# Kernel tuning notes

Hardware: AMD Instinct MI355X
Metric: run time of the kernel (lower is better)

Reference implementation:

```python
import jax, jax.numpy as jnp
import numpy as np

SHRINK_THRES = 0.0025
EPS = 1e-12  # F.normalize default eps


def _l2norm(v, axis=-1):
    return v / jnp.maximum(jnp.linalg.norm(v, axis=axis, keepdims=True), EPS)


def setup_inputs() -> dict:
    key = jax.random.key(0)
    ks = jax.random.split(key, 5)
    N, C, H, W = 16, 256, 64, 64
    mem_dim = 512
    x = jax.random.normal(ks[0], (N, C, H, W), dtype=jnp.float32)
    memory = jax.random.normal(ks[1], (mem_dim, C), dtype=jnp.float32) * 0.1
    memory = _l2norm(memory, axis=1)
    w1 = jax.random.normal(ks[2], (C, C // 2), dtype=jnp.float32) * (1.0 / np.sqrt(C))
    b1 = jnp.zeros((C // 2,), dtype=jnp.float32)
    w2 = jax.random.normal(ks[3], (C // 2, C), dtype=jnp.float32) * (1.0 / np.sqrt(C // 2))
    b2 = jnp.zeros((C,), dtype=jnp.float32)
    return {"x": x, "memory": memory, "w1": w1, "b1": b1, "w2": w2, "b2": b2}


def reference(x, memory, w1, b1, w2, b2):
    N, C, H, W = x.shape
    # [N,C,H,W] -> [N*H*W, C]
    x_flat = jnp.transpose(x, (0, 2, 3, 1)).reshape(-1, C)
    x_norm = _l2norm(x_flat, axis=1)
    # shared MLP over memory slots: Linear -> ReLU -> Linear -> ReLU
    m = jax.nn.relu(memory @ w1 + b1)
    m = jax.nn.relu(m @ w2 + b2)
    mem_norm = _l2norm(m, axis=1)  # [M, C]
    # cosine similarity + softmax over memory slots
    att = jax.nn.softmax(x_norm @ mem_norm.T, axis=1)  # [N*H*W, M]
    # hard shrink + L1 renormalization
    att = jax.nn.relu(att - SHRINK_THRES)
    att = att / jnp.maximum(jnp.sum(att, axis=1, keepdims=True), EPS)
    out_flat = att @ mem_norm  # [N*H*W, C]
    output = jnp.transpose(out_flat.reshape(N, H, W, C), (0, 3, 1, 2))
    att_map = jnp.transpose(att.reshape(N, H, W, -1), (0, 3, 1, 2))
    return output, att_map
```

## Files before the change

### kernel.cpp

```cpp
#include <hip/hip_runtime.h>
#include <hip/hip_bf16.h>

typedef _Float16 half8 __attribute__((ext_vector_type(8)));
typedef _Float16 half4v __attribute__((ext_vector_type(4)));
typedef float floatx4 __attribute__((ext_vector_type(4)));

#define C_DIM 256
#define M_DIM 512
#define HW 4096
#define TAU 0.0025f

__global__ __launch_bounds__(128) void prep_kernel(
    const float* __restrict__ memory, const float* __restrict__ w1,
    const float* __restrict__ b1, const float* __restrict__ w2,
    const float* __restrict__ b2,
    _Float16* __restrict__ mN, float* __restrict__ mN32)
{
  __shared__ float sm[256];
  __shared__ float sh[128];
  __shared__ float s_part[2];
  __shared__ float s_tot;
  const int r = blockIdx.x;
  const int t = threadIdx.x;
  sm[t]       = memory[r * C_DIM + t];
  sm[t + 128] = memory[r * C_DIM + t + 128];
  __syncthreads();
  float acc = b1[t];
#pragma unroll 8
  for (int c = 0; c < 256; ++c) acc = fmaf(sm[c], w1[c * 128 + t], acc);
  sh[t] = fmaxf(acc, 0.f);
  __syncthreads();
  float o0 = b2[t], o1 = b2[t + 128];
#pragma unroll 8
  for (int k = 0; k < 128; ++k) {
    float h = sh[k];
    o0 = fmaf(h, w2[k * 256 + t], o0);
    o1 = fmaf(h, w2[k * 256 + t + 128], o1);
  }
  o0 = fmaxf(o0, 0.f);
  o1 = fmaxf(o1, 0.f);
  float ss = o0 * o0 + o1 * o1;
#pragma unroll
  for (int off = 32; off >= 1; off >>= 1) ss += __shfl_down(ss, off);
  if ((t & 63) == 0) s_part[t >> 6] = ss;
  __syncthreads();
  if (t == 0) s_tot = s_part[0] + s_part[1];
  __syncthreads();
  const float inv = 1.f / fmaxf(sqrtf(s_tot), 1e-12f);
  const float v0 = o0 * inv, v1 = o1 * inv;
  mN[r * C_DIM + t]        = (_Float16)v0;
  mN[r * C_DIM + t + 128]  = (_Float16)v1;
  mN32[r * C_DIM + t]       = v0;
  mN32[r * C_DIM + t + 128] = v1;
}

#define MFMA16(a, b, c) __builtin_amdgcn_mfma_f32_16x16x32_f16(a, b, c, 0, 0, 0)

__global__ __launch_bounds__(512, 6) void main_kernel(
    const float* __restrict__ x,
    const _Float16* __restrict__ mN,
    const float* __restrict__ mN32,
    float* __restrict__ out, float* __restrict__ attmap)
{
  __shared__ _Float16 Xh[32][264];
  __shared__ int      s_lslot[32][120];
  __shared__ float    s_lval[32][120];
  __shared__ int      s_cnt[32];
  __shared__ float    s_sumsq[32];
  __shared__ float    s_sum1[32];
  __shared__ float    s_sum2[32];

  const int tid  = threadIdx.x;
  const int wave = tid >> 6;
  const int lane = tid & 63;
  const int q    = lane >> 4;
  const int c16  = lane & 15;
  const int g    = tid >> 3;
  const int pxq  = tid & 7;

  const int blk = blockIdx.x;
  const int img = blk >> 7;
  const int hw0 = (blk & 127) * 32;
  const float* __restrict__ xb = x + (size_t)img * C_DIM * HW + hw0;

  if (tid < 32) {
    s_sumsq[tid] = 0.f; s_sum1[tid] = 0.f; s_sum2[tid] = 0.f; s_cnt[tid] = 0;
  }
  __syncthreads();

  {
    floatx4 v[4];
#pragma unroll
    for (int i = 0; i < 4; ++i)
      v[i] = *(const floatx4*)(xb + (size_t)(4 * g + i) * HW + pxq * 4);
    float ps[4];
#pragma unroll
    for (int j = 0; j < 4; ++j) {
      const int p = pxq * 4 + j;
      half4v hv = {(_Float16)v[0][j], (_Float16)v[1][j], (_Float16)v[2][j], (_Float16)v[3][j]};
      *(half4v*)&Xh[p][4 * g] = hv;
      ps[j] = v[0][j] * v[0][j] + v[1][j] * v[1][j] + v[2][j] * v[2][j] + v[3][j] * v[3][j];
    }
#pragma unroll
    for (int off = 8; off < 64; off <<= 1)
#pragma unroll
      for (int j = 0; j < 4; ++j) ps[j] += __shfl_xor(ps[j], off);
    if ((lane >> 3) == 0) {
#pragma unroll
      for (int j = 0; j < 4; ++j) atomicAdd(&s_sumsq[4 * (lane & 7) + j], ps[j]);
    }
  }

  const _Float16* bp[4];
#pragma unroll
  for (int nt = 0; nt < 4; ++nt)
    bp[nt] = mN + (size_t)(wave * 64 + nt * 16 + c16) * C_DIM + q * 8;
  half8 bcur[4], bnxt[4];
#pragma unroll
  for (int nt = 0; nt < 4; ++nt) bcur[nt] = *(const half8*)bp[nt];

  __syncthreads();

  floatx4 acc[2][4];
#pragma unroll
  for (int mt = 0; mt < 2; ++mt)
#pragma unroll
    for (int nt = 0; nt < 4; ++nt) {
      floatx4 z = {0.f, 0.f, 0.f, 0.f};
      acc[mt][nt] = z;
    }
#pragma unroll
  for (int kb = 0; kb < 8; ++kb) {
    if (kb < 7) {
#pragma unroll
      for (int nt = 0; nt < 4; ++nt) bnxt[nt] = *(const half8*)(bp[nt] + (kb + 1) * 32);
    }
    const int k0 = kb * 32 + q * 8;
    const half8 ah0 = *(const half8*)&Xh[c16][k0];
    const half8 ah1 = *(const half8*)&Xh[16 + c16][k0];
#pragma unroll
    for (int nt = 0; nt < 4; ++nt) {
      acc[0][nt] = MFMA16(ah0, bcur[nt], acc[0][nt]);
      acc[1][nt] = MFMA16(ah1, bcur[nt], acc[1][nt]);
    }
#pragma unroll
    for (int nt = 0; nt < 4; ++nt) bcur[nt] = bnxt[nt];
  }

#pragma unroll
  for (int mt = 0; mt < 2; ++mt)
#pragma unroll
    for (int r = 0; r < 4; ++r) {
      const int m = mt * 16 + q * 4 + r;
      const float iv = 1.f / fmaxf(sqrtf(s_sumsq[m]), 1e-12f);
      float s = 0.f;
#pragma unroll
      for (int nt = 0; nt < 4; ++nt) {
        const float e = __expf(acc[mt][nt][r] * iv);
        acc[mt][nt][r] = e;
        s += e;
      }
      s += __shfl_xor(s, 1);
      s += __shfl_xor(s, 2);
      s += __shfl_xor(s, 4);
      s += __shfl_xor(s, 8);
      if (c16 == 0) atomicAdd(&s_sum1[m], s);
    }
  __syncthreads();

#pragma unroll
  for (int mt = 0; mt < 2; ++mt)
#pragma unroll
    for (int r = 0; r < 4; ++r) {
      const int m = mt * 16 + q * 4 + r;
      const float isum = 1.f / s_sum1[m];
      float s = 0.f;
#pragma unroll
      for (int nt = 0; nt < 4; ++nt) {
        const float tv = fmaxf(acc[mt][nt][r] * isum - TAU, 0.f);
        acc[mt][nt][r] = tv;
        s += tv;
      }
      s += __shfl_xor(s, 1);
      s += __shfl_xor(s, 2);
      s += __shfl_xor(s, 4);
      s += __shfl_xor(s, 8);
      if (c16 == 0) atomicAdd(&s_sum2[m], s);
    }
  __syncthreads();

#pragma unroll
  for (int mt = 0; mt < 2; ++mt) {
    float rs[4];
#pragma unroll
    for (int r = 0; r < 4; ++r)
      rs[r] = 1.f / fmaxf(s_sum2[mt * 16 + q * 4 + r], 1e-12f);
#pragma unroll
    for (int nt = 0; nt < 4; ++nt) {
      floatx4 a4 = acc[mt][nt];
      const int n = wave * 64 + nt * 16 + c16;
#pragma unroll
      for (int r = 0; r < 4; ++r) {
        a4[r] *= rs[r];
        if (a4[r] > 0.f) {
          const int m = mt * 16 + q * 4 + r;
          const int idx = atomicAdd(&s_cnt[m], 1);
          if (idx < 120) { s_lslot[m][idx] = n; s_lval[m][idx] = a4[r]; }
        }
      }
      acc[mt][nt] = a4;
    }
  }
  __syncthreads();

  const int px  = tid & 31;
  const int chc = tid >> 5;
  const int cn  = min(s_cnt[px], 120);
  floatx4 f[4] = {{0.f,0.f,0.f,0.f},{0.f,0.f,0.f,0.f},{0.f,0.f,0.f,0.f},{0.f,0.f,0.f,0.f}};
  for (int j = 0; j < cn; ++j) {
    const int slot = s_lslot[px][j];
    const float v  = s_lval[px][j];
    const floatx4* row = (const floatx4*)(mN32 + (size_t)slot * C_DIM + chc * 16);
#pragma unroll
    for (int u = 0; u < 4; ++u) f[u] += v * row[u];
  }

#pragma unroll
  for (int mt = 0; mt < 2; ++mt)
#pragma unroll
    for (int nt = 0; nt < 4; ++nt) {
      const int n = wave * 64 + nt * 16 + c16;
      *(floatx4*)(attmap + ((size_t)img * M_DIM + n) * HW + hw0 + mt * 16 + q * 4) =
          acc[mt][nt];
    }

#pragma unroll
  for (int cc = 0; cc < 16; ++cc)
    out[((size_t)img * C_DIM + chc * 16 + cc) * HW + hw0 + px] = f[cc >> 2][cc & 3];
}

extern "C" void kernel_launch(void* const* d_in, const int* in_sizes, int n_in,
                              void* d_out, int out_size, void* d_ws, size_t ws_size,
                              hipStream_t stream) {
  (void)in_sizes; (void)n_in; (void)out_size; (void)ws_size;
  const float* x      = (const float*)d_in[0];
  const float* memory = (const float*)d_in[1];
  const float* w1     = (const float*)d_in[2];
  const float* b1     = (const float*)d_in[3];
  const float* w2     = (const float*)d_in[4];
  const float* b2     = (const float*)d_in[5];
  float* out    = (float*)d_out;
  float* attmap = out + (size_t)16 * C_DIM * HW;

  _Float16* mN  = (_Float16*)d_ws;
  float*    mN32 = (float*)((char*)d_ws + (size_t)M_DIM * C_DIM * sizeof(_Float16));

  hipLaunchKernelGGL(prep_kernel, dim3(M_DIM), dim3(128), 0, stream,
                     memory, w1, b1, w2, b2, mN, mN32);
  hipLaunchKernelGGL(main_kernel, dim3(2048), dim3(512), 0, stream,
                     x, mN, mN32, out, attmap);
}
```

Before: 349.0 us.

## Double pixel tile per block, pack sparse attention list, use nontemporal stores

Each block now handles 64 pixels instead of 32, so every wave runs a 4x4 MFMA tile and each B-fragment load from memory is reused across twice as many rows. The launch shrinks to 1024 blocks. The sparse (slot, value) list is packed into one 32-bit word with an fp16 value to save LDS and offset the larger tile. The output and attention-map writes become nontemporal stores to avoid cache pollution. Costs are higher register pressure (launch bound drops to 4), fewer blocks for load balance, and fp16 rounding of the attention weights in the gather.

```diff
diff --git a/kernel.cpp b/kernel.cpp
--- a/kernel.cpp
+++ b/kernel.cpp
@@ -9,6 +9,7 @@
 #define M_DIM 512
 #define HW 4096
 #define TAU 0.0025f
+#define LCAP 120
 
 __global__ __launch_bounds__(128) void prep_kernel(
     const float* __restrict__ memory, const float* __restrict__ w1,
@@ -56,19 +57,18 @@
 
 #define MFMA16(a, b, c) __builtin_amdgcn_mfma_f32_16x16x32_f16(a, b, c, 0, 0, 0)
 
-__global__ __launch_bounds__(512, 6) void main_kernel(
+__global__ __launch_bounds__(512, 4) void main_kernel(
     const float* __restrict__ x,
     const _Float16* __restrict__ mN,
     const float* __restrict__ mN32,
     float* __restrict__ out, float* __restrict__ attmap)
 {
-  __shared__ _Float16 Xh[32][264];
-  __shared__ int      s_lslot[32][120];
-  __shared__ float    s_lval[32][120];
-  __shared__ int      s_cnt[32];
-  __shared__ float    s_sumsq[32];
-  __shared__ float    s_sum1[32];
-  __shared__ float    s_sum2[32];
+  __shared__ _Float16 Xh[64][264];
+  __shared__ unsigned s_list[64][LCAP];
+  __shared__ int      s_cnt[64];
+  __shared__ float    s_sumsq[64];
+  __shared__ float    s_sum1[64];
+  __shared__ float    s_sum2[64];
 
   const int tid  = threadIdx.x;
   const int wave = tid >> 6;
@@ -79,24 +79,25 @@
   const int pxq  = tid & 7;
 
   const int blk = blockIdx.x;
-  const int img = blk >> 7;
-  const int hw0 = (blk & 127) * 32;
+  const int img = blk >> 6;
+  const int hw0 = (blk & 63) * 64;
   const float* __restrict__ xb = x + (size_t)img * C_DIM * HW + hw0;
 
-  if (tid < 32) {
+  if (tid < 64) {
     s_sumsq[tid] = 0.f; s_sum1[tid] = 0.f; s_sum2[tid] = 0.f; s_cnt[tid] = 0;
   }
   __syncthreads();
 
-  {
+#pragma unroll
+  for (int h = 0; h < 2; ++h) {
     floatx4 v[4];
 #pragma unroll
     for (int i = 0; i < 4; ++i)
-      v[i] = *(const floatx4*)(xb + (size_t)(4 * g + i) * HW + pxq * 4);
+      v[i] = *(const floatx4*)(xb + (size_t)(4 * g + i) * HW + (pxq + 8 * h) * 4);
     float ps[4];
 #pragma unroll
     for (int j = 0; j < 4; ++j) {
-      const int p = pxq * 4 + j;
+      const int p = (pxq + 8 * h) * 4 + j;
       half4v hv = {(_Float16)v[0][j], (_Float16)v[1][j], (_Float16)v[2][j], (_Float16)v[3][j]};
       *(half4v*)&Xh[p][4 * g] = hv;
       ps[j] = v[0][j] * v[0][j] + v[1][j] * v[1][j] + v[2][j] * v[2][j] + v[3][j] * v[3][j];
@@ -107,7 +108,7 @@
       for (int j = 0; j < 4; ++j) ps[j] += __shfl_xor(ps[j], off);
     if ((lane >> 3) == 0) {
 #pragma unroll
-      for (int j = 0; j < 4; ++j) atomicAdd(&s_sumsq[4 * (lane & 7) + j], ps[j]);
+      for (int j = 0; j < 4; ++j) atomicAdd(&s_sumsq[4 * (lane & 7) + 32 * h + j], ps[j]);
     }
   }
 
@@ -121,9 +122,9 @@
 
   __syncthreads();
 
-  floatx4 acc[2][4];
-#pragma unroll
-  for (int mt = 0; mt < 2; ++mt)
+  floatx4 acc[4][4];
+#pragma unroll
+  for (int mt = 0; mt < 4; ++mt)
 #pragma unroll
     for (int nt = 0; nt < 4; ++nt) {
       floatx4 z = {0.f, 0.f, 0.f, 0.f};
@@ -136,19 +137,20 @@
       for (int nt = 0; nt < 4; ++nt) bnxt[nt] = *(const half8*)(bp[nt] + (kb + 1) * 32);
     }
     const int k0 = kb * 32 + q * 8;
-    const half8 ah0 = *(const half8*)&Xh[c16][k0];
-    const half8 ah1 = *(const half8*)&Xh[16 + c16][k0];
-#pragma unroll
-    for (int nt = 0; nt < 4; ++nt) {
-      acc[0][nt] = MFMA16(ah0, bcur[nt], acc[0][nt]);
-      acc[1][nt] = MFMA16(ah1, bcur[nt], acc[1][nt]);
-    }
+    half8 ah[4];
+#pragma unroll
+    for (int mt = 0; mt < 4; ++mt) ah[mt] = *(const half8*)&Xh[mt * 16 + c16][k0];
+#pragma unroll
+    for (int nt = 0; nt < 4; ++nt)
+#pragma unroll
+      for (int mt = 0; mt < 4; ++mt)
+        acc[mt][nt] = MFMA16(ah[mt], bcur[nt], acc[mt][nt]);
 #pragma unroll
     for (int nt = 0; nt < 4; ++nt) bcur[nt] = bnxt[nt];
   }
 
 #pragma unroll
-  for (int mt = 0; mt < 2; ++mt)
+  for (int mt = 0; mt < 4; ++mt)
 #pragma unroll
     for (int r = 0; r < 4; ++r) {
       const int m = mt * 16 + q * 4 + r;
@@ -169,7 +171,7 @@
   __syncthreads();
 
 #pragma unroll
-  for (int mt = 0; mt < 2; ++mt)
+  for (int mt = 0; mt < 4; ++mt)
 #pragma unroll
     for (int r = 0; r < 4; ++r) {
       const int m = mt * 16 + q * 4 + r;
@@ -190,7 +192,7 @@
   __syncthreads();
 
 #pragma unroll
-  for (int mt = 0; mt < 2; ++mt) {
+  for (int mt = 0; mt < 4; ++mt) {
     float rs[4];
 #pragma unroll
     for (int r = 0; r < 4; ++r)
@@ -198,14 +200,18 @@
 #pragma unroll
     for (int nt = 0; nt < 4; ++nt) {
       floatx4 a4 = acc[mt][nt];
-      const int n = wave * 64 + nt * 16 + c16;
+      const unsigned n = wave * 64 + nt * 16 + c16;
 #pragma unroll
       for (int r = 0; r < 4; ++r) {
         a4[r] *= rs[r];
         if (a4[r] > 0.f) {
           const int m = mt * 16 + q * 4 + r;
           const int idx = atomicAdd(&s_cnt[m], 1);
-          if (idx < 120) { s_lslot[m][idx] = n; s_lval[m][idx] = a4[r]; }
+          if (idx < LCAP) {
+            const unsigned short hb =
+                __builtin_bit_cast(unsigned short, (_Float16)a4[r]);
+            s_list[m][idx] = (n << 16) | (unsigned)hb;
+          }
         }
       }
       acc[mt][nt] = a4;
@@ -213,30 +219,35 @@
   }
   __syncthreads();
 
-  const int px  = tid & 31;
-  const int chc = tid >> 5;
-  const int cn  = min(s_cnt[px], 120);
-  floatx4 f[4] = {{0.f,0.f,0.f,0.f},{0.f,0.f,0.f,0.f},{0.f,0.f,0.f,0.f},{0.f,0.f,0.f,0.f}};
+  const int px  = lane;
+  const int chc = wave;
+  const int cn  = min(s_cnt[px], LCAP);
+  floatx4 f[8] = {{0.f,0.f,0.f,0.f},{0.f,0.f,0.f,0.f},{0.f,0.f,0.f,0.f},{0.f,0.f,0.f,0.f},
+                  {0.f,0.f,0.f,0.f},{0.f,0.f,0.f,0.f},{0.f,0.f,0.f,0.f},{0.f,0.f,0.f,0.f}};
   for (int j = 0; j < cn; ++j) {
-    const int slot = s_lslot[px][j];
-    const float v  = s_lval[px][j];
-    const floatx4* row = (const floatx4*)(mN32 + (size_t)slot * C_DIM + chc * 16);
-#pragma unroll
-    for (int u = 0; u < 4; ++u) f[u] += v * row[u];
-  }
-
-#pragma unroll
-  for (int mt = 0; mt < 2; ++mt)
+    const unsigned e = s_list[px][j];
+    const int slot   = (int)(e >> 16);
+    const float v    = (float)__builtin_bit_cast(_Float16, (unsigned short)(e & 0xffffu));
+    const floatx4* row = (const floatx4*)(mN32 + (size_t)slot * C_DIM + chc * 32);
+#pragma unroll
+    for (int u = 0; u < 8; ++u) f[u] += v * row[u];
+  }
+
+#pragma unroll
+  for (int mt = 0; mt < 4; ++mt)
 #pragma unroll
     for (int nt = 0; nt < 4; ++nt) {
       const int n = wave * 64 + nt * 16 + c16;
-      *(floatx4*)(attmap + ((size_t)img * M_DIM + n) * HW + hw0 + mt * 16 + q * 4) =
-          acc[mt][nt];
-    }
-
-#pragma unroll
-  for (int cc = 0; cc < 16; ++cc)
-    out[((size_t)img * C_DIM + chc * 16 + cc) * HW + hw0 + px] = f[cc >> 2][cc & 3];
+      __builtin_nontemporal_store(
+          acc[mt][nt],
+          (floatx4*)(attmap + ((size_t)img * M_DIM + n) * HW + hw0 + mt * 16 + q * 4));
+    }
+
+#pragma unroll
+  for (int cc = 0; cc < 32; ++cc)
+    __builtin_nontemporal_store(
+        f[cc >> 2][cc & 3],
+        out + ((size_t)img * C_DIM + chc * 32 + cc) * HW + hw0 + px);
 }
 
 extern "C" void kernel_launch(void* const* d_in, const int* in_sizes, int n_in,
@@ -252,11 +263,11 @@
   float* out    = (float*)d_out;
   float* attmap = out + (size_t)16 * C_DIM * HW;
 
-  _Float16* mN  = (_Float16*)d_ws;
+  _Float16* mN   = (_Float16*)d_ws;
   float*    mN32 = (float*)((char*)d_ws + (size_t)M_DIM * C_DIM * sizeof(_Float16));
 
   hipLaunchKernelGGL(prep_kernel, dim3(M_DIM), dim3(128), 0, stream,
                      memory, w1, b1, w2, b2, mN, mN32);
-  hipLaunchKernelGGL(main_kernel, dim3(2048), dim3(512), 0, stream,
+  hipLaunchKernelGGL(main_kernel, dim3(1024), dim3(512), 0, stream,
                      x, mN, mN32, out, attmap);
 }
```

Result: faster. 338.9 us (-2.9%).
